# Kernel optimization log

Measured on AMD Instinct MI355X. Metric: run time of the kernel, lower is better.

## Reference

```python
import jax, jax.numpy as jnp
import numpy as np

TILE = 128  # hardcoded tile size in tile_cache/untile_cache


def setup_inputs() -> dict:
    key = jax.random.key(0)
    k1, k2 = jax.random.split(key)
    B, H, D, T = 4, 8, 128, 64  # max_len = TILE * T = 8192
    # K stored tiled-transposed: (B, H, D, 128, num_tiles)
    k_cache = jax.random.normal(k1, (B, H, D, TILE, T), dtype=jnp.float32)
    # V stored tiled: (B, H, 128, num_tiles, D)
    v_cache = jax.random.normal(k2, (B, H, TILE, T, D), dtype=jnp.float32)
    return {"k_cache": k_cache, "v_cache": v_cache, "seq_len": 6144}


def reference(k_cache, v_cache, seq_len):
    # untile_cache, transposed=True: (B,H,D,128,T) -> (B,H,D,128*T)  [BHDS]
    B, H, D, tile, T = k_cache.shape
    k = k_cache.reshape(B, H, D, tile * T)
    # untile_cache, transposed=False: (B,H,128,T,D) -> (B,H,128*T,D)  [BHSD]
    Bv, Hv, tile_v, Tv, Dv = v_cache.shape
    v = v_cache.reshape(Bv, Hv, tile_v * Tv, Dv)
    # _slice_kv_cacheline, padding_side='right': slice [0, seq_len) on seq dim
    k = k[:, :, :, :seq_len]        # seq dim = 3 (transposed K)
    v = v[:, :, :seq_len, :]        # seq dim = 2
    # stack into a single output: transpose K back to BHSD to match V layout
    k_bhsd = jnp.swapaxes(k, 2, 3)  # (B,H,S,D)
    return jnp.stack([k_bhsd, v], axis=0)  # (2, B, H, seq_len, D)
```

## Files before the change

### kernel.cpp

```cpp
#include <hip/hip_runtime.h>


#define BH 32
#define DD 128
#define LDS_STRIDE 129

__global__ __launch_bounds__(256) void kv_repack(
    const float* __restrict__ kc, const float* __restrict__ vc,
    float* __restrict__ out,
    int S, int Sfull, int kBlocks, int vBlocksPerBH, int f4PerVBlock)
{
    __shared__ float lds[64 * LDS_STRIDE];

    const int bid = blockIdx.x;
    const int t = threadIdx.x;

    if (bid < kBlocks) {
        const int sTiles = S >> 7;
        const int perBH  = 2 * sTiles;
        const int bh     = bid / perBH;
        const int rem    = bid - bh * perBH;
        const int dTile  = rem / sTiles;
        const int sTile  = rem - dTile * sTiles;

        {
            const int s4 = t & 31;
            const int d0 = t >> 5;
            const float* src = kc
                + (size_t)(bh * DD + dTile * 64) * (size_t)Sfull
                + (size_t)(sTile << 7) + (s4 << 2);
#pragma unroll
            for (int i = 0; i < 8; ++i) {
                const int d = d0 + (i << 3);
                float4 v = *(const float4*)(src + (size_t)d * Sfull);
                float* L = &lds[d * LDS_STRIDE + (s4 << 2)];
                L[0] = v.x; L[1] = v.y; L[2] = v.z; L[3] = v.w;
            }
        }
        __syncthreads();

        {
            const int d4 = t & 15;
            const int r0 = t >> 4;
            float* dstBase = out
                + ((size_t)bh * S + (size_t)(sTile << 7)) * DD
                + dTile * 64 + (d4 << 2);
#pragma unroll
            for (int i = 0; i < 8; ++i) {
                const int sr = (i << 4) + r0;
                float4 v;
                v.x = lds[(4 * d4 + 0) * LDS_STRIDE + sr];
                v.y = lds[(4 * d4 + 1) * LDS_STRIDE + sr];
                v.z = lds[(4 * d4 + 2) * LDS_STRIDE + sr];
                v.w = lds[(4 * d4 + 3) * LDS_STRIDE + sr];
                *(float4*)(dstBase + (size_t)sr * DD) = v;
            }
        }
    } else {
        const int vb   = bid - kBlocks;
        const int bh   = vb / vBlocksPerBH;
        const int part = vb - bh * vBlocksPerBH;

        const size_t f4PerBHsrc = (size_t)Sfull * (DD / 4);
        const size_t f4PerBHdst = (size_t)S * (DD / 4);
        const size_t outVOff    = (size_t)BH * S * (DD / 4);

        const float4* src = (const float4*)vc + (size_t)bh * f4PerBHsrc
                            + (size_t)part * f4PerVBlock;
        float4* dst = (float4*)out + outVOff + (size_t)bh * f4PerBHdst
                      + (size_t)part * f4PerVBlock;

        for (int i = t; i < f4PerVBlock; i += 256)
            dst[i] = src[i];
    }
}

extern "C" void kernel_launch(void* const* d_in, const int* in_sizes, int n_in,
                              void* d_out, int out_size, void* d_ws, size_t ws_size,
                              hipStream_t stream) {
    const float* kc = (const float*)d_in[0];
    const float* vc = (const float*)d_in[1];
    float* out = (float*)d_out;

    const int S     = out_size / (2 * BH * DD);
    const int Sfull = in_sizes[0] / (BH * DD);

    const int sTiles        = S >> 7;
    const int kBlocks       = BH * 2 * sTiles;
    const int vBlocksPerBH  = sTiles;
    const int f4PerVBlock   = (S * (DD / 4)) / vBlocksPerBH;
    const int vBlocks       = BH * vBlocksPerBH;

    dim3 grid(kBlocks + vBlocks);
    dim3 block(256);
    kv_repack<<<grid, block, 0, stream>>>(kc, vc, out, S, Sfull,
                                          kBlocks, vBlocksPerBH, f4PerVBlock);
}
```

Baseline: 357.4 us.

## Use direct global-to-LDS loads with XOR swizzle and nontemporal streaming copies

The K transpose path now loads tiles straight into LDS with global_load_lds 16-byte transfers. It replaces the padded stride with an XOR-swizzled layout so the transposed LDS reads avoid bank conflicts. Output stores and the V copy use nontemporal loads and stores, and the V copy is unrolled by four to keep more loads in flight. This targets register round-trips and cache pollution in a bandwidth-bound copy, but depends on the swizzle indexing matching the wave-wide LDS write layout of global_load_lds.

Result: no change. 353.9 us (-1.0%).

```diff
diff --git a/kernel.cpp b/kernel.cpp
--- a/kernel.cpp
+++ b/kernel.cpp
@@ -3,14 +3,22 @@
 
 #define BH 32
 #define DD 128
-#define LDS_STRIDE 129
+
+typedef float f4 __attribute__((ext_vector_type(4)));
+
+__device__ __forceinline__ void gload_lds16(const float* g, float* l) {
+    __builtin_amdgcn_global_load_lds(
+        (const __attribute__((address_space(1))) void*)g,
+        (__attribute__((address_space(3))) void*)l,
+        16, 0, 0);
+}
 
 __global__ __launch_bounds__(256) void kv_repack(
     const float* __restrict__ kc, const float* __restrict__ vc,
     float* __restrict__ out,
     int S, int Sfull, int kBlocks, int vBlocksPerBH, int f4PerVBlock)
 {
-    __shared__ float lds[64 * LDS_STRIDE];
+    __shared__ float lds[64 * DD];
 
     const int bid = blockIdx.x;
     const int t = threadIdx.x;
@@ -23,18 +31,22 @@
         const int dTile  = rem / sTiles;
         const int sTile  = rem - dTile * sTiles;
 
+        const int wave = t >> 6;
+        const int lane = t & 63;
+
         {
-            const int s4 = t & 31;
-            const int d0 = t >> 5;
-            const float* src = kc
+            const float* rowbase = kc
                 + (size_t)(bh * DD + dTile * 64) * (size_t)Sfull
-                + (size_t)(sTile << 7) + (s4 << 2);
+                + (size_t)(sTile << 7);
+            const int c  = lane & 31;
+            const int dh = lane >> 5;
 #pragma unroll
             for (int i = 0; i < 8; ++i) {
-                const int d = d0 + (i << 3);
-                float4 v = *(const float4*)(src + (size_t)d * Sfull);
-                float* L = &lds[d * LDS_STRIDE + (s4 << 2)];
-                L[0] = v.x; L[1] = v.y; L[2] = v.z; L[3] = v.w;
+                const int dbase = (wave << 4) + (i << 1);
+                const int d  = dbase + dh;
+                const int s4 = c ^ (d >> 2);
+                gload_lds16(rowbase + (size_t)d * Sfull + (s4 << 2),
+                            &lds[dbase << 7]);
             }
         }
         __syncthreads();
@@ -47,13 +59,15 @@
                 + dTile * 64 + (d4 << 2);
 #pragma unroll
             for (int i = 0; i < 8; ++i) {
-                const int sr = (i << 4) + r0;
-                float4 v;
-                v.x = lds[(4 * d4 + 0) * LDS_STRIDE + sr];
-                v.y = lds[(4 * d4 + 1) * LDS_STRIDE + sr];
-                v.z = lds[(4 * d4 + 2) * LDS_STRIDE + sr];
-                v.w = lds[(4 * d4 + 3) * LDS_STRIDE + sr];
-                *(float4*)(dstBase + (size_t)sr * DD) = v;
+                const int sr  = (i << 4) + r0;
+                const int col = (((sr >> 2) ^ d4) << 2) + (sr & 3);
+                const int base = (d4 << 9) + col;
+                f4 v;
+                v.x = lds[base];
+                v.y = lds[base + DD];
+                v.z = lds[base + 2 * DD];
+                v.w = lds[base + 3 * DD];
+                __builtin_nontemporal_store(v, (f4*)(dstBase + (size_t)sr * DD));
             }
         }
     } else {
@@ -65,13 +79,27 @@
         const size_t f4PerBHdst = (size_t)S * (DD / 4);
         const size_t outVOff    = (size_t)BH * S * (DD / 4);
 
-        const float4* src = (const float4*)vc + (size_t)bh * f4PerBHsrc
-                            + (size_t)part * f4PerVBlock;
-        float4* dst = (float4*)out + outVOff + (size_t)bh * f4PerBHdst
-                      + (size_t)part * f4PerVBlock;
+        const f4* src = (const f4*)vc + (size_t)bh * f4PerBHsrc
+                        + (size_t)part * f4PerVBlock;
+        f4* dst = (f4*)out + outVOff + (size_t)bh * f4PerBHdst
+                  + (size_t)part * f4PerVBlock;
 
-        for (int i = t; i < f4PerVBlock; i += 256)
-            dst[i] = src[i];
+        const int n = f4PerVBlock;
+        int j = t;
+        for (; j + 768 < n; j += 1024) {
+            f4 a0 = __builtin_nontemporal_load(src + j);
+            f4 a1 = __builtin_nontemporal_load(src + j + 256);
+            f4 a2 = __builtin_nontemporal_load(src + j + 512);
+            f4 a3 = __builtin_nontemporal_load(src + j + 768);
+            __builtin_nontemporal_store(a0, dst + j);
+            __builtin_nontemporal_store(a1, dst + j + 256);
+            __builtin_nontemporal_store(a2, dst + j + 512);
+            __builtin_nontemporal_store(a3, dst + j + 768);
+        }
+        for (; j < n; j += 256) {
+            f4 a = __builtin_nontemporal_load(src + j);
+            __builtin_nontemporal_store(a, dst + j);
+        }
     }
 }
 
```
